# Kernel optimization log

Measured on AMD Instinct MI355X. Metric: run time of the kernel, lower is better.

## Reference

```python
import jax
import jax.numpy as jnp
from jax import lax
import numpy as np

EMBED_DIM = 768
NUM_HEADS = 12
BATCH = 8
SEQ = 1024
EPS = 1e-07
QK_QBIT = 8
QK_KBIT = 8
AV_ABIT = 8
AV_VBIT = 8
PROJ_WBIT = 8
PROJ_XBIT = 8
SCALE = EMBED_DIM ** (-0.5)  # module uses embed_dim, not head_dim


def _ste(hard, soft):
    # straight-through estimator: forward = hard, backward grad = d(soft)
    return soft + lax.stop_gradient(hard - soft)


def fake_quant_signed(x, bit):
    # _quantize_signed_matrix_train: sign/abs, global-max scaling, STE clamp + round
    sign = lax.stop_gradient(jnp.sign(x))
    a = jnp.abs(x)
    scaling = lax.stop_gradient(jnp.max(a)) + EPS
    y = a / scaling
    y = _ste(jnp.clip(y, 0.0, 1.0), y)          # Clamp.apply (STE)
    levels = 2.0 ** (bit - 1.0) - 1.0
    y = _ste(jnp.round(y * levels) / levels, y)  # Round.apply (STE)
    return y * scaling * sign


def fake_quant_unsigned(x, bit):
    # _quantize_unsigned_matrix_train
    scaling = lax.stop_gradient(jnp.max(x)) + EPS
    y = x / scaling
    y = _ste(jnp.clip(y, 0.0, 1.0), y)
    levels = 2.0 ** bit - 1.0
    y = _ste(jnp.round(y * levels) / levels, y)
    return y * scaling


def asim_linear(x, w, b, wbit, xbit):
    # ASiMLinear in 'Train' mode with signed_act=True: fake-quantize activation
    # and weight, dense matmul, trim_noise=0 -> no perturbation.
    xq = fake_quant_signed(x, xbit)
    wq = fake_quant_signed(w, wbit)
    return jnp.einsum('bnc,oc->bno', xq, wq) + b


def setup_inputs() -> dict:
    key = jax.random.key(0)
    k_x, k_qw, k_qb, k_pw, k_pb = jax.random.split(key, 5)
    x = jax.random.normal(k_x, (BATCH, SEQ, EMBED_DIM), dtype=jnp.float32)
    s = 1.0 / np.sqrt(EMBED_DIM)
    qkv_w = jax.random.normal(k_qw, (3 * EMBED_DIM, EMBED_DIM), dtype=jnp.float32) * s
    qkv_b = jax.random.normal(k_qb, (3 * EMBED_DIM,), dtype=jnp.float32) * 0.01
    proj_w = jax.random.normal(k_pw, (EMBED_DIM, EMBED_DIM), dtype=jnp.float32) * s
    proj_b = jax.random.normal(k_pb, (EMBED_DIM,), dtype=jnp.float32) * 0.01
    return {'x': x, 'qkv_w': qkv_w, 'qkv_b': qkv_b, 'proj_w': proj_w, 'proj_b': proj_b}


def reference(x, qkv_w, qkv_b, proj_w, proj_b):
    B, N, C = x.shape
    H = NUM_HEADS
    D = C // H
    # qkv projection (ASiMLinear, Train mode)
    qkv = asim_linear(x, qkv_w, qkv_b, PROJ_WBIT, PROJ_XBIT)      # [B, N, 3C]
    qkv = qkv.reshape(B, N, 3, H, D).transpose(2, 0, 3, 1, 4)      # [3, B, H, N, D]
    q, k, v = qkv[0], qkv[1], qkv[2]
    # _qk_train: fake-quantize q and k^T, matmul (trim_noise=0 -> no perturb)
    qq = fake_quant_signed(q, QK_QBIT)
    kq = fake_quant_signed(jnp.swapaxes(k, -2, -1), QK_KBIT)
    attn = jnp.einsum('bhnd,bhdm->bhnm', qq, kq) * SCALE           # [B, H, N, N]
    attn = jax.nn.softmax(attn, axis=-1)
    # dropout ratio 0.0 -> identity
    # _av_train: unsigned fake-quant of attention, signed fake-quant of v
    aq = fake_quant_unsigned(attn, AV_ABIT)
    vq = fake_quant_signed(v, AV_VBIT)
    out = jnp.einsum('bhnm,bhmd->bhnd', aq, vq)                    # [B, H, N, D]
    out = out.transpose(0, 2, 1, 3).reshape(B, N, C)
    # output projection (ASiMLinear, Train mode)
    out = asim_linear(out, proj_w, proj_b, PROJ_WBIT, PROJ_XBIT)
    return out
```

## Files before the change

kernel.cpp:

```cpp
#include <hip/hip_runtime.h>
#include <hip/hip_bf16.h>
#include <cstdint>
#include <cstddef>

#define B_    8
#define SEQ_  1024
#define C_    768
#define H_    12
#define D_    64
#define TC_   2304
#define M_    8192
#define EPS_  1e-7f
#define SCALE_ 0.036084391824351615f

typedef __attribute__((ext_vector_type(8))) short bf16x8;
typedef __attribute__((ext_vector_type(4))) float f32x4;
typedef __attribute__((ext_vector_type(4))) int   i32x4;

__device__ __forceinline__ void expand16(int4 raw, int4& lo, int4& hi) {
  union { int4 v; signed char c[16]; } u; u.v = raw;
  unsigned short s[16];
  #pragma unroll
  for (int j = 0; j < 16; ++j) {
    float f = (float)(int)u.c[j];
    s[j] = (unsigned short)(__float_as_uint(f) >> 16);
  }
  lo = *(const int4*)&s[0]; hi = *(const int4*)&s[8];
}

__device__ __forceinline__ int8_t quant1(float v, float s) {
  float y = fminf(fabsf(v) / s, 1.0f);
  int q = (int)rintf(y * 127.0f);
  return (int8_t)(v < 0.f ? -q : q);
}

__global__ void k_init(float* g) {
  if (threadIdx.x == 0) {
    g[0]=0.f; g[1]=0.f; g[2]=0.f; g[3]=0.f; g[4]=0.f; g[5]=0.f;
    g[6]=3.402823466e+38f;
    g[7]=0.f;
  }
}

__global__ __launch_bounds__(256) void k_absmax_fused(const float4* __restrict__ x,
                                                      const float4* __restrict__ w1,
                                                      const float4* __restrict__ w2,
                                                      float* g) {
  __shared__ float red[4];
  const int blk = blockIdx.x;
  const float4* p; unsigned n4; float* gout; int b0, nb;
  if (blk < 384)      { p = x;  n4 = 1572864u; gout = &g[0]; b0 = 0;   nb = 384; }
  else if (blk < 480) { p = w1; n4 = 442368u;  gout = &g[1]; b0 = 384; nb = 96;  }
  else                { p = w2; n4 = 147456u;  gout = &g[2]; b0 = 480; nb = 48;  }
  float m = 0.f;
  for (unsigned i = (unsigned)(blk - b0) * 256u + threadIdx.x; i < n4; i += (unsigned)nb * 256u) {
    float4 v = p[i];
    m = fmaxf(m, fmaxf(fmaxf(fabsf(v.x), fabsf(v.y)), fmaxf(fabsf(v.z), fabsf(v.w))));
  }
  #pragma unroll
  for (int off = 32; off; off >>= 1) m = fmaxf(m, __shfl_xor(m, off));
  if ((threadIdx.x & 63) == 0) red[threadIdx.x >> 6] = m;
  __syncthreads();
  if (threadIdx.x == 0) {
    m = fmaxf(fmaxf(red[0], red[1]), fmaxf(red[2], red[3]));
    atomicMax((unsigned int*)gout, __float_as_uint(m));
  }
}

__device__ __forceinline__ void quant_seg4(const float4* __restrict__ in, unsigned n4, float s,
                                           int8_t* __restrict__ out, unsigned i0, unsigned stride) {
  for (unsigned i = i0; i < n4; i += stride) {
    float4 v = in[i];
    union { unsigned int u; int8_t c[4]; } pk;
    pk.c[0] = quant1(v.x, s);
    pk.c[1] = quant1(v.y, s);
    pk.c[2] = quant1(v.z, s);
    pk.c[3] = quant1(v.w, s);
    *(unsigned int*)&out[(size_t)i * 4] = pk.u;
  }
}
__global__ __launch_bounds__(256) void k_quant_fused(const float4* __restrict__ x,
                                                     const float4* __restrict__ w1,
                                                     const float4* __restrict__ w2,
                                                     const float* __restrict__ g,
                                                     int8_t* __restrict__ xq,
                                                     int8_t* __restrict__ wq,
                                                     int8_t* __restrict__ pw) {
  const int blk = blockIdx.x;
  if (blk < 1536)      quant_seg4(x,  1572864u, g[0] + EPS_, xq, (unsigned)blk * 256u + threadIdx.x, 1536u * 256u);
  else if (blk < 1968) quant_seg4(w1, 442368u,  g[1] + EPS_, wq, (unsigned)(blk - 1536) * 256u + threadIdx.x, 432u * 256u);
  else                 quant_seg4(w2, 147456u,  g[2] + EPS_, pw, (unsigned)(blk - 1968) * 256u + threadIdx.x, 144u * 256u);
}

__global__ __launch_bounds__(256) void k_quant_i8(const float4* __restrict__ in, unsigned n4,
                                                  const float* __restrict__ gmax,
                                                  int8_t* __restrict__ out) {
  const float s = *gmax + EPS_;
  quant_seg4(in, n4, s, out, blockIdx.x * blockDim.x + threadIdx.x, gridDim.x * blockDim.x);
}

__global__ __launch_bounds__(256) void k_gemm8i(const int8_t* __restrict__ A,
                                                const int8_t* __restrict__ Bt,
                                                const float* __restrict__ bias,
                                                float* __restrict__ C,
                                                int Mn, int Nn, int Kn,
                                                const float* __restrict__ sA, const float* __restrict__ sB,
                                                float* pmax, int partDiv) {
  __shared__ int8_t As[4][128][16];
  __shared__ int8_t Bs[4][128][16];
  const int tid = threadIdx.x;
  int flat = blockIdx.y * gridDim.x + blockIdx.x;
  int chunk = (gridDim.x * gridDim.y) >> 3;
  int nf = (flat & 7) * chunk + (flat >> 3);
  const int n0 = (nf % gridDim.x) * 128, m0 = (nf / gridDim.x) * 128;
  const int wid = tid >> 6, lane = tid & 63;
  const int wr = wid >> 1, wc = wid & 1;
  const int lrow = lane & 15;
  const int lslot = lane >> 4;
  i32x4 acc[4][4] = {};
  const int srow = tid & 127;
  const int slot0 = tid >> 7;
  const int8_t* ga = A  + (size_t)(m0 + srow) * Kn + slot0 * 16;
  const int8_t* gb = Bt + (size_t)(n0 + srow) * Kn + slot0 * 16;
  const int nt = Kn >> 6;
  int4 ra0_0 = *(const int4*)(ga);
  int4 ra1_0 = *(const int4*)(ga + 32);
  int4 rb0_0 = *(const int4*)(gb);
  int4 rb1_0 = *(const int4*)(gb + 32);
  int4 ra0_1 = *(const int4*)(ga + 64);
  int4 ra1_1 = *(const int4*)(ga + 96);
  int4 rb0_1 = *(const int4*)(gb + 64);
  int4 rb1_1 = *(const int4*)(gb + 96);
  #define KSTEP(SET, T)                                                        \
    if (T) __syncthreads();                                                    \
    *(int4*)&As[slot0][srow][0]     = ra0_##SET;                               \
    *(int4*)&As[slot0 + 2][srow][0] = ra1_##SET;                               \
    *(int4*)&Bs[slot0][srow][0]     = rb0_##SET;                               \
    *(int4*)&Bs[slot0 + 2][srow][0] = rb1_##SET;                               \
    if ((T) + 2 < nt) {                                                        \
      const int ko_ = ((T) + 2) << 6;                                          \
      ra0_##SET = *(const int4*)(ga + ko_);                                    \
      ra1_##SET = *(const int4*)(ga + ko_ + 32);                               \
      rb0_##SET = *(const int4*)(gb + ko_);                                    \
      rb1_##SET = *(const int4*)(gb + ko_ + 32);                               \
    }                                                                          \
    __syncthreads();                                                           \
    {                                                                          \
      i32x4 af[4], bfr[4];                                                     \
      _Pragma("unroll")                                                        \
      for (int i = 0; i < 4; ++i) af[i]  = *(const i32x4*)&As[lslot][wr * 64 + i * 16 + lrow][0]; \
      _Pragma("unroll")                                                        \
      for (int j = 0; j < 4; ++j) bfr[j] = *(const i32x4*)&Bs[lslot][wc * 64 + j * 16 + lrow][0]; \
      _Pragma("unroll")                                                        \
      for (int i = 0; i < 4; ++i)                                              \
        _Pragma("unroll")                                                      \
        for (int j = 0; j < 4; ++j)                                            \
          acc[i][j] = __builtin_amdgcn_mfma_i32_16x16x64_i8(af[i], bfr[j], acc[i][j], 0, 0, 0); \
    }
  for (int t = 0; t < nt; t += 2) {
    KSTEP(0, t)
    KSTEP(1, t + 1)
  }
  #undef KSTEP
  const float alpha = (sA[0] + EPS_) * (sB[0] + EPS_) * (1.0f / 16129.0f);
  const int orow = (lane >> 4) << 2;
  float amax = 0.f;
  #pragma unroll
  for (int i = 0; i < 4; ++i) {
    #pragma unroll
    for (int j = 0; j < 4; ++j) {
      int col = n0 + wc * 64 + j * 16 + lrow;
      float bc = bias[col];
      #pragma unroll
      for (int rr = 0; rr < 4; ++rr) {
        int row = m0 + wr * 64 + i * 16 + orow + rr;
        float val = (float)acc[i][j][rr] * alpha + bc;
        __builtin_nontemporal_store(val, &C[(size_t)row * Nn + col]);
        amax = fmaxf(amax, fabsf(val));
      }
    }
  }
  if (pmax) {
    #pragma unroll
    for (int off = 32; off; off >>= 1) amax = fmaxf(amax, __shfl_xor(amax, off));
    if (lane == 0) atomicMax((unsigned int*)&pmax[n0 / partDiv], __float_as_uint(amax));
  }
}

__global__ __launch_bounds__(256) void k_quant_heads(const float* __restrict__ qkvf, const float* __restrict__ g,
                                                     int8_t* __restrict__ qo, int8_t* __restrict__ ko,
                                                     int8_t* __restrict__ vT) {
  __shared__ float vt[64][65];
  const int bh = blockIdx.x >> 4, nt = blockIdx.x & 15;
  const int b = bh / 12, h = bh % 12;
  const int n0 = nt * 64;
  const int tid = threadIdx.x;
  const float s0 = g[3] + EPS_, s1 = g[4] + EPS_, s2 = g[5] + EPS_;
  const int r = tid >> 2, dc = tid & 3;
  const size_t mrow = (size_t)(b * 1024 + n0 + r) * 2304;
  union { int4 v; int8_t c[16]; } pk;
  {
    const float4* src = (const float4*)(qkvf + mrow + h * 64 + dc * 16);
    float4 v0 = src[0], v1 = src[1], v2 = src[2], v3 = src[3];
    pk.c[0]=quant1(v0.x,s0); pk.c[1]=quant1(v0.y,s0); pk.c[2]=quant1(v0.z,s0); pk.c[3]=quant1(v0.w,s0);
    pk.c[4]=quant1(v1.x,s0); pk.c[5]=quant1(v1.y,s0); pk.c[6]=quant1(v1.z,s0); pk.c[7]=quant1(v1.w,s0);
    pk.c[8]=quant1(v2.x,s0); pk.c[9]=quant1(v2.y,s0); pk.c[10]=quant1(v2.z,s0); pk.c[11]=quant1(v2.w,s0);
    pk.c[12]=quant1(v3.x,s0); pk.c[13]=quant1(v3.y,s0); pk.c[14]=quant1(v3.z,s0); pk.c[15]=quant1(v3.w,s0);
    *(int4*)&qo[((size_t)bh * 1024 + n0 + r) * 64 + dc * 16] = pk.v;
  }
  {
    const float4* src = (const float4*)(qkvf + mrow + 768 + h * 64 + dc * 16);
    float4 v0 = src[0], v1 = src[1], v2 = src[2], v3 = src[3];
    pk.c[0]=quant1(v0.x,s1); pk.c[1]=quant1(v0.y,s1); pk.c[2]=quant1(v0.z,s1); pk.c[3]=quant1(v0.w,s1);
    pk.c[4]=quant1(v1.x,s1); pk.c[5]=quant1(v1.y,s1); pk.c[6]=quant1(v1.z,s1); pk.c[7]=quant1(v1.w,s1);
    pk.c[8]=quant1(v2.x,s1); pk.c[9]=quant1(v2.y,s1); pk.c[10]=quant1(v2.z,s1); pk.c[11]=quant1(v2.w,s1);
    pk.c[12]=quant1(v3.x,s1); pk.c[13]=quant1(v3.y,s1); pk.c[14]=quant1(v3.z,s1); pk.c[15]=quant1(v3.w,s1);
    *(int4*)&ko[((size_t)bh * 1024 + n0 + r) * 64 + dc * 16] = pk.v;
  }
  {
    const float4* src = (const float4*)(qkvf + mrow + 1536 + h * 64 + dc * 16);
    float4 v0 = src[0], v1 = src[1], v2 = src[2], v3 = src[3];
    vt[dc*16+ 0][r]=v0.x; vt[dc*16+ 1][r]=v0.y; vt[dc*16+ 2][r]=v0.z; vt[dc*16+ 3][r]=v0.w;
    vt[dc*16+ 4][r]=v1.x; vt[dc*16+ 5][r]=v1.y; vt[dc*16+ 6][r]=v1.z; vt[dc*16+ 7][r]=v1.w;
    vt[dc*16+ 8][r]=v2.x; vt[dc*16+ 9][r]=v2.y; vt[dc*16+10][r]=v2.z; vt[dc*16+11][r]=v2.w;
    vt[dc*16+12][r]=v3.x; vt[dc*16+13][r]=v3.y; vt[dc*16+14][r]=v3.z; vt[dc*16+15][r]=v3.w;
  }
  __syncthreads();
  {
    const int d = tid >> 2, nc = tid & 3;
    #pragma unroll
    for (int e = 0; e < 16; ++e) pk.c[e] = quant1(vt[d][nc * 16 + e], s2);
    *(int4*)&vT[((size_t)bh * 64 + d) * 1024 + n0 + nc * 16] = pk.v;
  }
}

__global__ __launch_bounds__(256) void k_attn_stats_mfma(
    const int8_t* __restrict__ qi8, const int8_t* __restrict__ ki8,
    const float* __restrict__ g, float* __restrict__ rowmax, float* __restrict__ denomv,
    unsigned int* __restrict__ gminden) {
  __shared__ int8_t Ks[4][64][16];
  __shared__ float red[4];
  const int bh = blockIdx.x >> 4, rt = blockIdx.x & 15;
  const int tid = threadIdx.x, w = tid >> 6, lane = tid & 63;
  const int lrow = lane & 15, lslot = lane >> 4;
  const int8_t* qbase = qi8 + (size_t)bh * 65536;
  const int8_t* kbase = ki8 + (size_t)bh * 65536;
  const i32x4 qf = *(const i32x4*)(qbase + (size_t)(rt*64 + w*16 + lrow) * 64 + lslot * 16);
  const float qkScale = (g[3] + EPS_) * (g[4] + EPS_) * (1.0f / 16129.0f) * SCALE_;
  float m = -3.0e38f, den = 0.f;
  const int krow = tid & 63, kslot = tid >> 6;
  int4 kraw = *(const int4*)(kbase + (size_t)krow * 64 + kslot * 16);
  for (int t = 0; t < 16; ++t) {
    __syncthreads();
    *(int4*)&Ks[kslot][krow][0] = kraw;
    if (t < 15)
      kraw = *(const int4*)(kbase + (size_t)(t + 1) * 4096 + (size_t)krow * 64 + kslot * 16);
    __syncthreads();
    i32x4 acc[4] = {};
    #pragma unroll
    for (int j = 0; j < 4; ++j) {
      i32x4 kf = *(const i32x4*)&Ks[lslot][j * 16 + lrow][0];
      acc[j] = __builtin_amdgcn_mfma_i32_16x16x64_i8(kf, qf, acc[j], 0, 0, 0);
    }
    float mnew = m;
    #pragma unroll
    for (int j = 0; j < 4; ++j)
      #pragma unroll
      for (int rr = 0; rr < 4; ++rr)
        mnew = fmaxf(mnew, (float)acc[j][rr] * qkScale);
    float d = den * __expf(m - mnew);
    #pragma unroll
    for (int j = 0; j < 4; ++j)
      #pragma unroll
      for (int rr = 0; rr < 4; ++rr)
        d += __expf((float)acc[j][rr] * qkScale - mnew);
    den = d; m = mnew;
  }
  #pragma unroll
  for (int off = 16; off <= 32; off <<= 1) {
    float mo = __shfl_xor(m, off);
    float doo = __shfl_xor(den, off);
    float mg = fmaxf(m, mo);
    den = den * __expf(m - mg) + doo * __expf(mo - mg);
    m = mg;
  }
  if (lane < 16) {
    size_t rg = (size_t)bh * 1024 + rt * 64 + w * 16 + lane;
    rowmax[rg] = m;
    denomv[rg] = den;
  }
  float bm = den;
  #pragma unroll
  for (int off = 1; off < 16; off <<= 1) bm = fminf(bm, __shfl_xor(bm, off));
  if (lane == 0) red[w] = bm;
  __syncthreads();
  if (tid == 0)
    atomicMin(gminden, __float_as_uint(fminf(fminf(red[0], red[1]), fminf(red[2], red[3]))));
}

__global__ __launch_bounds__(256) void k_attn_pv_mfma(
    const int8_t* __restrict__ qi8, const int8_t* __restrict__ ki8, const int8_t* __restrict__ vti8,
    const float* __restrict__ g, const unsigned int* __restrict__ gminden,
    const float* __restrict__ rowmax, const float* __restrict__ denomv,
    float* __restrict__ aof, float* __restrict__ gamax) {
  __shared__ int8_t Ks[4][64][16];
  __shared__ unsigned short Vs[64 * 64];
  __shared__ unsigned short Ps[64 * 64];
  __shared__ float red[4];
  const int bh = blockIdx.x >> 4, rt = blockIdx.x & 15;
  const int b = bh / 12, h = bh % 12;
  const int tid = threadIdx.x, w = tid >> 6, lane = tid & 63;
  const int lrow = lane & 15, lslot = lane >> 4, lko = lslot << 3;
  const int8_t* qbase = qi8 + (size_t)bh * 65536;
  const int8_t* kbase = ki8 + (size_t)bh * 65536;
  const int8_t* vbase = vti8 + (size_t)bh * 65536;
  const i32x4 qf = *(const i32x4*)(qbase + (size_t)(rt*64 + w*16 + lrow) * 64 + lslot * 16);
  const float qkScale = (g[3] + EPS_) * (g[4] + EPS_) * (1.0f / 16129.0f) * SCALE_;
  const float minden = __uint_as_float(*gminden);
  const float sa = 1.0f / minden + EPS_;
  const float invSa = 1.0f / sa;
  const float sv = g[5] + EPS_;
  const float pvScale = sa * sv * (1.0f / 32385.0f);
  const float rm  = rowmax[(size_t)bh * 1024 + rt * 64 + w * 16 + lrow];
  const float ivd = 1.0f / denomv[(size_t)bh * 1024 + rt * 64 + w * 16 + lrow];
  f32x4 accO[4] = {};
  const int krow = tid & 63, kslot = tid >> 6;
  const int srow = tid >> 2, sc = tid & 3;
  const int sx = (srow & 7) << 4;
  int4 kraw = *(const int4*)(kbase + (size_t)krow * 64 + kslot * 16);
  int4 vraw = *(const int4*)(vbase + (size_t)srow * 1024 + sc * 16);
  for (int t = 0; t < 16; ++t) {
    __syncthreads();
    *(int4*)&Ks[kslot][krow][0] = kraw;
    {
      int4 lo, hi;
      int bb = srow * 128 + sc * 32;
      expand16(vraw, lo, hi);
      *(int4*)((char*)Vs + ( bb       ^ sx)) = lo;
      *(int4*)((char*)Vs + ((bb + 16) ^ sx)) = hi;
    }
    if (t < 15) {
      kraw = *(const int4*)(kbase + (size_t)(t + 1) * 4096 + (size_t)krow * 64 + kslot * 16);
      vraw = *(const int4*)(vbase + (size_t)srow * 1024 + (t + 1) * 64 + sc * 16);
    }
    __syncthreads();
    i32x4 acc[4] = {};
    #pragma unroll
    for (int j = 0; j < 4; ++j) {
      i32x4 kf = *(const i32x4*)&Ks[lslot][j * 16 + lrow][0];
      acc[j] = __builtin_amdgcn_mfma_i32_16x16x64_i8(kf, qf, acc[j], 0, 0, 0);
    }
    const int q = w * 16 + lrow;
    const int kb = lslot << 2;
    #pragma unroll
    for (int j = 0; j < 4; ++j) {
      float a0 = rintf(fminf(__expf((float)acc[j][0] * qkScale - rm) * ivd * invSa, 1.0f) * 255.0f);
      float a1 = rintf(fminf(__expf((float)acc[j][1] * qkScale - rm) * ivd * invSa, 1.0f) * 255.0f);
      float a2 = rintf(fminf(__expf((float)acc[j][2] * qkScale - rm) * ivd * invSa, 1.0f) * 255.0f);
      float a3 = rintf(fminf(__expf((float)acc[j][3] * qkScale - rm) * ivd * invSa, 1.0f) * 255.0f);
      uint2 pk;
      pk.x = (__float_as_uint(a0) >> 16) | ((__float_as_uint(a1) >> 16) << 16);
      pk.y = (__float_as_uint(a2) >> 16) | ((__float_as_uint(a3) >> 16) << 16);
      int byteoff = (q * 128 + (j * 16 + kb) * 2) ^ ((q & 7) << 4);
      *(uint2*)((char*)Ps + byteoff) = pk;
    }
    #pragma unroll
    for (int ks = 0; ks < 2; ++ks) {
      bf16x8 pf = *(const bf16x8*)((const char*)Ps + ((q * 128 + (ks*32 + lko) * 2) ^ ((q & 7) << 4)));
      #pragma unroll
      for (int j = 0; j < 4; ++j) {
        int row = j * 16 + lrow;
        bf16x8 vf = *(const bf16x8*)((const char*)Vs + ((row * 128 + (ks*32 + lko) * 2) ^ ((row & 7) << 4)));
        accO[j] = __builtin_amdgcn_mfma_f32_16x16x32_bf16(pf, vf, accO[j], 0, 0, 0);
      }
    }
  }
  float amax = 0.f;
  #pragma unroll
  for (int j = 0; j < 4; ++j) {
    int d = j * 16 + lrow;
    #pragma unroll
    for (int rr = 0; rr < 4; ++rr) {
      int row = rt * 64 + w * 16 + (lane >> 4) * 4 + rr;
      float val = accO[j][rr] * pvScale;
      aof[((size_t)(b * 1024 + row)) * 768 + h * 64 + d] = val;
      amax = fmaxf(amax, fabsf(val));
    }
  }
  #pragma unroll
  for (int off = 1; off < 64; off <<= 1) amax = fmaxf(amax, __shfl_xor(amax, off));
  if (lane == 0) red[w] = amax;
  __syncthreads();
  if (tid == 0)
    atomicMax((unsigned int*)gamax, __float_as_uint(fmaxf(fmaxf(red[0], red[1]), fmaxf(red[2], red[3]))));
}

extern "C" void kernel_launch(void* const* d_in, const int* in_sizes, int n_in,
                              void* d_out, int out_size, void* d_ws, size_t ws_size,
                              hipStream_t stream) {
  const float* x      = (const float*)d_in[0];
  const float* qkv_w  = (const float*)d_in[1];
  const float* qkv_b  = (const float*)d_in[2];
  const float* proj_w = (const float*)d_in[3];
  const float* proj_b = (const float*)d_in[4];
  float* out = (float*)d_out;

  char* w = (char*)d_ws;
  float*          g      = (float*)(w + 0);
  float*          rowmax = (float*)(w + 256);
  float*          denomv = (float*)(w + 393472);
  int8_t*         qi8    = (int8_t*)(w + 786688);
  int8_t*         ki8    = (int8_t*)(w + 7078144);
  int8_t*         vT     = (int8_t*)(w + 13369600);
  int8_t*         pw8    = (int8_t*)(w + 19661056);
  int8_t*         xq8    = (int8_t*)(w + 20840704);
  int8_t*         wq8    = (int8_t*)(w + 33423616);
  float*          qkvf   = (float*)(w + 36962560);
  float*          aof    = (float*)(w + 36962560);
  int8_t*         aob8   = (int8_t*)(w + 62128384);

  hipLaunchKernelGGL(k_init, dim3(1), dim3(64), 0, stream, g);

  hipLaunchKernelGGL(k_absmax_fused, dim3(528), dim3(256), 0, stream,
                     (const float4*)x, (const float4*)qkv_w, (const float4*)proj_w, g);

  hipLaunchKernelGGL(k_quant_fused, dim3(2112), dim3(256), 0, stream,
                     (const float4*)x, (const float4*)qkv_w, (const float4*)proj_w, g, xq8, wq8, pw8);

  hipLaunchKernelGGL(k_gemm8i, dim3(TC_ / 128, M_ / 128), dim3(256), 0, stream,
                     xq8, wq8, qkv_b, qkvf, M_, TC_, C_, &g[0], &g[1], &g[3], 768);

  hipLaunchKernelGGL(k_quant_heads, dim3(1536), dim3(256), 0, stream, qkvf, g, qi8, ki8, vT);

  hipLaunchKernelGGL(k_attn_stats_mfma, dim3(1536), dim3(256), 0, stream,
                     qi8, ki8, g, rowmax, denomv, (unsigned int*)&g[6]);
  hipLaunchKernelGGL(k_attn_pv_mfma, dim3(1536), dim3(256), 0, stream,
                     qi8, ki8, vT, g, (const unsigned int*)&g[6], rowmax, denomv, aof, &g[7]);

  hipLaunchKernelGGL(k_quant_i8, dim3(2048), dim3(256), 0, stream,
                     (const float4*)aof, 1572864u, &g[7], aob8);

  hipLaunchKernelGGL(k_gemm8i, dim3(C_ / 128, M_ / 128), dim3(256), 0, stream,
                     aob8, pw8, proj_b, out, M_, C_, C_, &g[7], &g[2], (float*)nullptr, 1);

  (void)in_sizes; (void)n_in; (void)out_size; (void)ws_size;
}
```

Measured before the change: 228.1 us.

## Fuse activation int8 quantization into GEMM A-tile loads, dropping separate quant passes

Both int8 GEMMs now read fp32 activations directly and quantize them to int8 while staging the A tile into shared memory. This removes the separate quantize kernels for x and the attention output, along with their int8 intermediate buffers and extra global round trips. In exchange, the GEMM reads four times more A bytes and loses the two-deep register prefetch for A, since A loads are now issued in the same iteration they are used. The output stores also switch from nontemporal to normal stores.

```diff
diff --git a/kernel.cpp b/kernel.cpp
--- a/kernel.cpp
+++ b/kernel.cpp
@@ -32,6 +32,14 @@
   float y = fminf(fabsf(v) / s, 1.0f);
   int q = (int)rintf(y * 127.0f);
   return (int8_t)(v < 0.f ? -q : q);
+}
+__device__ __forceinline__ int4 qpack16(float4 a, float4 b, float4 c, float4 d, float s) {
+  union { int4 v; int8_t q[16]; } pk;
+  pk.q[0]=quant1(a.x,s);  pk.q[1]=quant1(a.y,s);  pk.q[2]=quant1(a.z,s);  pk.q[3]=quant1(a.w,s);
+  pk.q[4]=quant1(b.x,s);  pk.q[5]=quant1(b.y,s);  pk.q[6]=quant1(b.z,s);  pk.q[7]=quant1(b.w,s);
+  pk.q[8]=quant1(c.x,s);  pk.q[9]=quant1(c.y,s);  pk.q[10]=quant1(c.z,s); pk.q[11]=quant1(c.w,s);
+  pk.q[12]=quant1(d.x,s); pk.q[13]=quant1(d.y,s); pk.q[14]=quant1(d.z,s); pk.q[15]=quant1(d.w,s);
+  return pk.v;
 }
 
 __global__ void k_init(float* g) {
@@ -79,33 +87,23 @@
     *(unsigned int*)&out[(size_t)i * 4] = pk.u;
   }
 }
-__global__ __launch_bounds__(256) void k_quant_fused(const float4* __restrict__ x,
-                                                     const float4* __restrict__ w1,
+__global__ __launch_bounds__(256) void k_quant_fused(const float4* __restrict__ w1,
                                                      const float4* __restrict__ w2,
                                                      const float* __restrict__ g,
-                                                     int8_t* __restrict__ xq,
                                                      int8_t* __restrict__ wq,
                                                      int8_t* __restrict__ pw) {
   const int blk = blockIdx.x;
-  if (blk < 1536)      quant_seg4(x,  1572864u, g[0] + EPS_, xq, (unsigned)blk * 256u + threadIdx.x, 1536u * 256u);
-  else if (blk < 1968) quant_seg4(w1, 442368u,  g[1] + EPS_, wq, (unsigned)(blk - 1536) * 256u + threadIdx.x, 432u * 256u);
-  else                 quant_seg4(w2, 147456u,  g[2] + EPS_, pw, (unsigned)(blk - 1968) * 256u + threadIdx.x, 144u * 256u);
-}
-
-__global__ __launch_bounds__(256) void k_quant_i8(const float4* __restrict__ in, unsigned n4,
-                                                  const float* __restrict__ gmax,
-                                                  int8_t* __restrict__ out) {
-  const float s = *gmax + EPS_;
-  quant_seg4(in, n4, s, out, blockIdx.x * blockDim.x + threadIdx.x, gridDim.x * blockDim.x);
-}
-
-__global__ __launch_bounds__(256) void k_gemm8i(const int8_t* __restrict__ A,
-                                                const int8_t* __restrict__ Bt,
-                                                const float* __restrict__ bias,
-                                                float* __restrict__ C,
-                                                int Mn, int Nn, int Kn,
-                                                const float* __restrict__ sA, const float* __restrict__ sB,
-                                                float* pmax, int partDiv) {
+  if (blk < 432) quant_seg4(w1, 442368u, g[1] + EPS_, wq, (unsigned)blk * 256u + threadIdx.x, 432u * 256u);
+  else           quant_seg4(w2, 147456u, g[2] + EPS_, pw, (unsigned)(blk - 432) * 256u + threadIdx.x, 144u * 256u);
+}
+
+__global__ __launch_bounds__(256) void k_gemm8i_qa(const float* __restrict__ Af,
+                                                   const int8_t* __restrict__ Bt,
+                                                   const float* __restrict__ bias,
+                                                   float* __restrict__ C,
+                                                   int Mn, int Nn, int Kn,
+                                                   const float* __restrict__ sA, const float* __restrict__ sB,
+                                                   float* pmax, int partDiv) {
   __shared__ int8_t As[4][128][16];
   __shared__ int8_t Bs[4][128][16];
   const int tid = threadIdx.x;
@@ -120,48 +118,38 @@
   i32x4 acc[4][4] = {};
   const int srow = tid & 127;
   const int slot0 = tid >> 7;
-  const int8_t* ga = A  + (size_t)(m0 + srow) * Kn + slot0 * 16;
-  const int8_t* gb = Bt + (size_t)(n0 + srow) * Kn + slot0 * 16;
+  const float sq = sA[0] + EPS_;
+  const float*  gaf = Af + (size_t)(m0 + srow) * Kn + slot0 * 16;
+  const int8_t* gb  = Bt + (size_t)(n0 + srow) * Kn + slot0 * 16;
   const int nt = Kn >> 6;
-  int4 ra0_0 = *(const int4*)(ga);
-  int4 ra1_0 = *(const int4*)(ga + 32);
-  int4 rb0_0 = *(const int4*)(gb);
-  int4 rb1_0 = *(const int4*)(gb + 32);
-  int4 ra0_1 = *(const int4*)(ga + 64);
-  int4 ra1_1 = *(const int4*)(ga + 96);
-  int4 rb0_1 = *(const int4*)(gb + 64);
-  int4 rb1_1 = *(const int4*)(gb + 96);
-  #define KSTEP(SET, T)                                                        \
-    if (T) __syncthreads();                                                    \
-    *(int4*)&As[slot0][srow][0]     = ra0_##SET;                               \
-    *(int4*)&As[slot0 + 2][srow][0] = ra1_##SET;                               \
-    *(int4*)&Bs[slot0][srow][0]     = rb0_##SET;                               \
-    *(int4*)&Bs[slot0 + 2][srow][0] = rb1_##SET;                               \
-    if ((T) + 2 < nt) {                                                        \
-      const int ko_ = ((T) + 2) << 6;                                          \
-      ra0_##SET = *(const int4*)(ga + ko_);                                    \
-      ra1_##SET = *(const int4*)(ga + ko_ + 32);                               \
-      rb0_##SET = *(const int4*)(gb + ko_);                                    \
-      rb1_##SET = *(const int4*)(gb + ko_ + 32);                               \
-    }                                                                          \
-    __syncthreads();                                                           \
-    {                                                                          \
-      i32x4 af[4], bfr[4];                                                     \
-      _Pragma("unroll")                                                        \
-      for (int i = 0; i < 4; ++i) af[i]  = *(const i32x4*)&As[lslot][wr * 64 + i * 16 + lrow][0]; \
-      _Pragma("unroll")                                                        \
-      for (int j = 0; j < 4; ++j) bfr[j] = *(const i32x4*)&Bs[lslot][wc * 64 + j * 16 + lrow][0]; \
-      _Pragma("unroll")                                                        \
-      for (int i = 0; i < 4; ++i)                                              \
-        _Pragma("unroll")                                                      \
-        for (int j = 0; j < 4; ++j)                                            \
-          acc[i][j] = __builtin_amdgcn_mfma_i32_16x16x64_i8(af[i], bfr[j], acc[i][j], 0, 0, 0); \
-    }
-  for (int t = 0; t < nt; t += 2) {
-    KSTEP(0, t)
-    KSTEP(1, t + 1)
-  }
-  #undef KSTEP
+  int4 rb0 = *(const int4*)(gb);
+  int4 rb1 = *(const int4*)(gb + 32);
+  for (int t = 0; t < nt; ++t) {
+    const float4* pa = (const float4*)(gaf + (size_t)t * 64);
+    float4 x0 = pa[0], x1 = pa[1], x2 = pa[2],  x3 = pa[3];
+    float4 y0 = pa[8], y1 = pa[9], y2 = pa[10], y3 = pa[11];
+    if (t) __syncthreads();
+    *(int4*)&As[slot0][srow][0]     = qpack16(x0, x1, x2, x3, sq);
+    *(int4*)&As[slot0 + 2][srow][0] = qpack16(y0, y1, y2, y3, sq);
+    *(int4*)&Bs[slot0][srow][0]     = rb0;
+    *(int4*)&Bs[slot0 + 2][srow][0] = rb1;
+    if (t + 1 < nt) {
+      const int ko = (t + 1) << 6;
+      rb0 = *(const int4*)(gb + ko);
+      rb1 = *(const int4*)(gb + ko + 32);
+    }
+    __syncthreads();
+    i32x4 af[4], bfr[4];
+    #pragma unroll
+    for (int i = 0; i < 4; ++i) af[i]  = *(const i32x4*)&As[lslot][wr * 64 + i * 16 + lrow][0];
+    #pragma unroll
+    for (int j = 0; j < 4; ++j) bfr[j] = *(const i32x4*)&Bs[lslot][wc * 64 + j * 16 + lrow][0];
+    #pragma unroll
+    for (int i = 0; i < 4; ++i)
+      #pragma unroll
+      for (int j = 0; j < 4; ++j)
+        acc[i][j] = __builtin_amdgcn_mfma_i32_16x16x64_i8(af[i], bfr[j], acc[i][j], 0, 0, 0);
+  }
   const float alpha = (sA[0] + EPS_) * (sB[0] + EPS_) * (1.0f / 16129.0f);
   const int orow = (lane >> 4) << 2;
   float amax = 0.f;
@@ -175,7 +163,7 @@
       for (int rr = 0; rr < 4; ++rr) {
         int row = m0 + wr * 64 + i * 16 + orow + rr;
         float val = (float)acc[i][j][rr] * alpha + bc;
-        __builtin_nontemporal_store(val, &C[(size_t)row * Nn + col]);
+        C[(size_t)row * Nn + col] = val;
         amax = fmaxf(amax, fabsf(val));
       }
     }
@@ -198,24 +186,15 @@
   const float s0 = g[3] + EPS_, s1 = g[4] + EPS_, s2 = g[5] + EPS_;
   const int r = tid >> 2, dc = tid & 3;
   const size_t mrow = (size_t)(b * 1024 + n0 + r) * 2304;
-  union { int4 v; int8_t c[16]; } pk;
   {
     const float4* src = (const float4*)(qkvf + mrow + h * 64 + dc * 16);
-    float4 v0 = src[0], v1 = src[1], v2 = src[2], v3 = src[3];
-    pk.c[0]=quant1(v0.x,s0); pk.c[1]=quant1(v0.y,s0); pk.c[2]=quant1(v0.z,s0); pk.c[3]=quant1(v0.w,s0);
-    pk.c[4]=quant1(v1.x,s0); pk.c[5]=quant1(v1.y,s0); pk.c[6]=quant1(v1.z,s0); pk.c[7]=quant1(v1.w,s0);
-    pk.c[8]=quant1(v2.x,s0); pk.c[9]=quant1(v2.y,s0); pk.c[10]=quant1(v2.z,s0); pk.c[11]=quant1(v2.w,s0);
-    pk.c[12]=quant1(v3.x,s0); pk.c[13]=quant1(v3.y,s0); pk.c[14]=quant1(v3.z,s0); pk.c[15]=quant1(v3.w,s0);
-    *(int4*)&qo[((size_t)bh * 1024 + n0 + r) * 64 + dc * 16] = pk.v;
+    *(int4*)&qo[((size_t)bh * 1024 + n0 + r) * 64 + dc * 16] =
+        qpack16(src[0], src[1], src[2], src[3], s0);
   }
   {
     const float4* src = (const float4*)(qkvf + mrow + 768 + h * 64 + dc * 16);
-    float4 v0 = src[0], v1 = src[1], v2 = src[2], v3 = src[3];
-    pk.c[0]=quant1(v0.x,s1); pk.c[1]=quant1(v0.y,s1); pk.c[2]=quant1(v0.z,s1); pk.c[3]=quant1(v0.w,s1);
-    pk.c[4]=quant1(v1.x,s1); pk.c[5]=quant1(v1.y,s1); pk.c[6]=quant1(v1.z,s1); pk.c[7]=quant1(v1.w,s1);
-    pk.c[8]=quant1(v2.x,s1); pk.c[9]=quant1(v2.y,s1); pk.c[10]=quant1(v2.z,s1); pk.c[11]=quant1(v2.w,s1);
-    pk.c[12]=quant1(v3.x,s1); pk.c[13]=quant1(v3.y,s1); pk.c[14]=quant1(v3.z,s1); pk.c[15]=quant1(v3.w,s1);
-    *(int4*)&ko[((size_t)bh * 1024 + n0 + r) * 64 + dc * 16] = pk.v;
+    *(int4*)&ko[((size_t)bh * 1024 + n0 + r) * 64 + dc * 16] =
+        qpack16(src[0], src[1], src[2], src[3], s1);
   }
   {
     const float4* src = (const float4*)(qkvf + mrow + 1536 + h * 64 + dc * 16);
@@ -228,6 +207,7 @@
   __syncthreads();
   {
     const int d = tid >> 2, nc = tid & 3;
+    union { int4 v; int8_t c[16]; } pk;
     #pragma unroll
     for (int e = 0; e < 16; ++e) pk.c[e] = quant1(vt[d][nc * 16 + e], s2);
     *(int4*)&vT[((size_t)bh * 64 + d) * 1024 + n0 + nc * 16] = pk.v;
@@ -413,22 +393,20 @@
   int8_t*         ki8    = (int8_t*)(w + 7078144);
   int8_t*         vT     = (int8_t*)(w + 13369600);
   int8_t*         pw8    = (int8_t*)(w + 19661056);
-  int8_t*         xq8    = (int8_t*)(w + 20840704);
   int8_t*         wq8    = (int8_t*)(w + 33423616);
   float*          qkvf   = (float*)(w + 36962560);
   float*          aof    = (float*)(w + 36962560);
-  int8_t*         aob8   = (int8_t*)(w + 62128384);
 
   hipLaunchKernelGGL(k_init, dim3(1), dim3(64), 0, stream, g);
 
   hipLaunchKernelGGL(k_absmax_fused, dim3(528), dim3(256), 0, stream,
                      (const float4*)x, (const float4*)qkv_w, (const float4*)proj_w, g);
 
-  hipLaunchKernelGGL(k_quant_fused, dim3(2112), dim3(256), 0, stream,
-                     (const float4*)x, (const float4*)qkv_w, (const float4*)proj_w, g, xq8, wq8, pw8);
-
-  hipLaunchKernelGGL(k_gemm8i, dim3(TC_ / 128, M_ / 128), dim3(256), 0, stream,
-                     xq8, wq8, qkv_b, qkvf, M_, TC_, C_, &g[0], &g[1], &g[3], 768);
+  hipLaunchKernelGGL(k_quant_fused, dim3(576), dim3(256), 0, stream,
+                     (const float4*)qkv_w, (const float4*)proj_w, g, wq8, pw8);
+
+  hipLaunchKernelGGL(k_gemm8i_qa, dim3(TC_ / 128, M_ / 128), dim3(256), 0, stream,
+                     x, wq8, qkv_b, qkvf, M_, TC_, C_, &g[0], &g[1], &g[3], 768);
 
   hipLaunchKernelGGL(k_quant_heads, dim3(1536), dim3(256), 0, stream, qkvf, g, qi8, ki8, vT);
 
@@ -437,11 +415,8 @@
   hipLaunchKernelGGL(k_attn_pv_mfma, dim3(1536), dim3(256), 0, stream,
                      qi8, ki8, vT, g, (const unsigned int*)&g[6], rowmax, denomv, aof, &g[7]);
 
-  hipLaunchKernelGGL(k_quant_i8, dim3(2048), dim3(256), 0, stream,
-                     (const float4*)aof, 1572864u, &g[7], aob8);
-
-  hipLaunchKernelGGL(k_gemm8i, dim3(C_ / 128, M_ / 128), dim3(256), 0, stream,
-                     aob8, pw8, proj_b, out, M_, C_, C_, &g[7], &g[2], (float*)nullptr, 1);
+  hipLaunchKernelGGL(k_gemm8i_qa, dim3(C_ / 128, M_ / 128), dim3(256), 0, stream,
+                     aof, pw8, proj_b, out, M_, C_, C_, &g[7], &g[2], (float*)nullptr, 1);
 
   (void)in_sizes; (void)n_in; (void)out_size; (void)ws_size;
 }
```

After: 281.3 us. 1.23x slower.
